# Kernel tuning notes

Measured on AMD Instinct MI355X. Metric: run time of the kernel, lower is better.

Reference implementation:

```python
import jax, jax.numpy as jnp
import numpy as np

EPS = 1e-15
BALL_EPS = 1e-5  # geoopt-style clamp away from the ball boundary


def expmap0(u):
    # Poincare ball (curvature -1): expmap0(u) = tanh(||u||) * u / ||u||
    n = jnp.linalg.norm(u, axis=-1, keepdims=True)
    n = jnp.maximum(n, EPS)
    return jnp.tanh(n) * u / n


def setup_inputs() -> dict:
    key = jax.random.key(0)
    k1, k2, k3 = jax.random.split(key, 3)
    B, H, D, L = 32768, 768, 384, 128
    cls_output = jax.random.normal(k1, (B, H), dtype=jnp.float32)
    W_proj = jax.random.normal(k2, (H, D), dtype=jnp.float32) * 0.02
    b_proj = jnp.zeros((D,), dtype=jnp.float32)
    # class prototypes: uniform(-0.1, 0.1) then expmap0, as in __init__
    tangent = jax.random.uniform(k3, (L, D), dtype=jnp.float32, minval=-0.1, maxval=0.1)
    poincare_weight = expmap0(tangent)
    return {"cls_output": cls_output, "W_proj": W_proj, "b_proj": b_proj,
            "poincare_weight": poincare_weight}


def reference(cls_output, W_proj, b_proj, poincare_weight):
    # projection (dropout is identity in eval mode)
    projected = cls_output @ W_proj + b_proj            # [B, D]
    x = expmap0(projected)                              # [B, D] points in ball
    y = poincare_weight                                 # [L, D] class reps in ball
    # Poincare distance for all (B, L) pairs, fused via dot products:
    # ||(-x) mobius+ y||^2 = ||x - y||^2 / (1 - 2<x,y> + ||x||^2 ||y||^2)
    x2 = jnp.sum(x * x, axis=-1)                        # [B]
    y2 = jnp.sum(y * y, axis=-1)                        # [L]
    xy = x @ y.T                                        # [B, L]
    sq_diff = x2[:, None] + y2[None, :] - 2.0 * xy      # ||x - y||^2
    denom = 1.0 - 2.0 * xy + x2[:, None] * y2[None, :]
    ratio = jnp.clip(sq_diff / denom, 0.0, (1.0 - BALL_EPS) ** 2)
    dist = 2.0 * jnp.arctanh(jnp.sqrt(ratio))           # [B, L]
    logits = -dist
    return logits, x
```

## Files before the change

kernel.cpp:

```cpp
#include <hip/hip_runtime.h>

typedef __attribute__((ext_vector_type(8))) short bf16x8;
typedef __attribute__((ext_vector_type(16))) float f32x16;

__device__ __forceinline__ unsigned short f2b(float f) {
  unsigned x = __builtin_bit_cast(unsigned, f);
  x += 0x7fffu + ((x >> 16) & 1u);
  return (unsigned short)(x >> 16);
}

__global__ __launch_bounds__(256) void k_prep(const float* __restrict__ W,
                                              const float* __restrict__ Y,
                                              unsigned short* __restrict__ Wt,
                                              unsigned short* __restrict__ Ybf,
                                              float* __restrict__ y2) {
  __shared__ unsigned short sT[64][72];
  int b = blockIdx.x;
  if (b < 72) {
    int bk = (b % 12) * 64, bn = (b / 12) * 64;
    int c = threadIdx.x & 63, rr = threadIdx.x >> 6;
#pragma unroll
    for (int i = 0; i < 16; i++) {
      int row = rr * 16 + i;
      sT[row][c] = f2b(W[(size_t)(bk + row) * 384 + bn + c]);
    }
    __syncthreads();
#pragma unroll
    for (int i = 0; i < 16; i++) {
      int row = rr * 16 + i;
      Wt[(size_t)(bn + row) * 768 + bk + c] = sT[c][row];
    }
  } else {
    int t = threadIdx.x;
    for (int i = t; i < 12288; i += 256) {
      float4 v = ((const float4*)Y)[i];
      ushort4 o;
      o.x = f2b(v.x); o.y = f2b(v.y); o.z = f2b(v.z); o.w = f2b(v.w);
      ((ushort4*)Ybf)[i] = o;
    }
    if (t < 128) {
      const float4* row = (const float4*)(Y + (size_t)t * 384);
      float s = 0.f;
#pragma unroll
      for (int j = 0; j < 96; j++) {
        float4 v = row[j];
        s += v.x * v.x + v.y * v.y + v.z * v.z + v.w * v.w;
      }
      y2[t] = s;
    }
  }
}

#define LDS1 72

__global__ __launch_bounds__(512, 2) void k_proj(const float* __restrict__ cls,
                                                 const unsigned short* __restrict__ Wt,
                                                 const float* __restrict__ bias,
                                                 float* __restrict__ xout,
                                                 float* __restrict__ x2out) {
  __shared__ unsigned short sA[128 * LDS1];
  __shared__ unsigned short sW[384 * LDS1];
  __shared__ float rs[128][4];
  __shared__ float sF[128];

  const int tid = threadIdx.x;
  const int bm = blockIdx.x * 128;
  const int wave = tid >> 6, lane = tid & 63;
  const int r = lane & 31, h = lane >> 5;
  const int rg = wave & 1, cg = wave >> 1;

  f32x16 acc[2][3];
#pragma unroll
  for (int i = 0; i < 2; i++)
#pragma unroll
    for (int j = 0; j < 3; j++)
#pragma unroll
      for (int e = 0; e < 16; e++) acc[i][j][e] = 0.f;

  for (int k0 = 0; k0 < 768; k0 += 64) {
    __syncthreads();
#pragma unroll
    for (int c = tid; c < 1024; c += 512) {
      int row = c >> 3, kc = c & 7;
      const float* src = cls + (size_t)(bm + row) * 768 + k0 + kc * 8;
      float4 f0 = *(const float4*)(src);
      float4 f1 = *(const float4*)(src + 4);
      uint4 p;
      p.x = (unsigned)f2b(f0.x) | ((unsigned)f2b(f0.y) << 16);
      p.y = (unsigned)f2b(f0.z) | ((unsigned)f2b(f0.w) << 16);
      p.z = (unsigned)f2b(f1.x) | ((unsigned)f2b(f1.y) << 16);
      p.w = (unsigned)f2b(f1.z) | ((unsigned)f2b(f1.w) << 16);
      *(uint4*)(sA + row * LDS1 + kc * 8) = p;
    }
#pragma unroll
    for (int c = tid; c < 3072; c += 512) {
      int row = c >> 3, kc = c & 7;
      *(uint4*)(sW + row * LDS1 + kc * 8) =
          *(const uint4*)(Wt + (size_t)row * 768 + k0 + kc * 8);
    }
    __syncthreads();
#pragma unroll
    for (int sub = 0; sub < 4; sub++) {
      const int kk = sub * 16 + h * 8;
      bf16x8 a0 = *(const bf16x8*)(sA + (rg * 64 + r) * LDS1 + kk);
      bf16x8 a1 = *(const bf16x8*)(sA + (rg * 64 + 32 + r) * LDS1 + kk);
      bf16x8 b0 = *(const bf16x8*)(sW + (cg * 96 + r) * LDS1 + kk);
      bf16x8 b1 = *(const bf16x8*)(sW + (cg * 96 + 32 + r) * LDS1 + kk);
      bf16x8 b2 = *(const bf16x8*)(sW + (cg * 96 + 64 + r) * LDS1 + kk);
      acc[0][0] = __builtin_amdgcn_mfma_f32_32x32x16_bf16(a0, b0, acc[0][0], 0, 0, 0);
      acc[0][1] = __builtin_amdgcn_mfma_f32_32x32x16_bf16(a0, b1, acc[0][1], 0, 0, 0);
      acc[0][2] = __builtin_amdgcn_mfma_f32_32x32x16_bf16(a0, b2, acc[0][2], 0, 0, 0);
      acc[1][0] = __builtin_amdgcn_mfma_f32_32x32x16_bf16(a1, b0, acc[1][0], 0, 0, 0);
      acc[1][1] = __builtin_amdgcn_mfma_f32_32x32x16_bf16(a1, b1, acc[1][1], 0, 0, 0);
      acc[1][2] = __builtin_amdgcn_mfma_f32_32x32x16_bf16(a1, b2, acc[1][2], 0, 0, 0);
    }
  }

  float bcol[3];
#pragma unroll
  for (int j = 0; j < 3; j++) bcol[j] = bias[cg * 96 + j * 32 + r];

#pragma unroll
  for (int i = 0; i < 2; i++) {
#pragma unroll
    for (int reg = 0; reg < 16; reg++) {
      float s = 0.f;
#pragma unroll
      for (int j = 0; j < 3; j++) {
        float v = acc[i][j][reg] + bcol[j];
        acc[i][j][reg] = v;
        s += v * v;
      }
      s += __shfl_xor(s, 1);
      s += __shfl_xor(s, 2);
      s += __shfl_xor(s, 4);
      s += __shfl_xor(s, 8);
      s += __shfl_xor(s, 16);
      if (r == 0) {
        int rowl = rg * 64 + i * 32 + (reg & 3) + 8 * (reg >> 2) + 4 * h;
        rs[rowl][cg] = s;
      }
    }
  }
  __syncthreads();
  if (tid < 128) {
    float n2 = rs[tid][0] + rs[tid][1] + rs[tid][2] + rs[tid][3];
    float n = fmaxf(sqrtf(n2), 1e-15f);
    float f = tanhf(n) / n;
    sF[tid] = f;
    x2out[bm + tid] = n2 * f * f;
  }
  __syncthreads();
#pragma unroll
  for (int i = 0; i < 2; i++) {
#pragma unroll
    for (int reg = 0; reg < 16; reg++) {
      int rowl = rg * 64 + i * 32 + (reg & 3) + 8 * (reg >> 2) + 4 * h;
      float f = sF[rowl];
#pragma unroll
      for (int j = 0; j < 3; j++) {
        xout[(size_t)(bm + rowl) * 384 + cg * 96 + j * 32 + r] = acc[i][j][reg] * f;
      }
    }
  }
}

#define LDS2 136

__global__ __launch_bounds__(512, 4) void k_logits(const float* __restrict__ X,
                                                   const float* __restrict__ x2,
                                                   const unsigned short* __restrict__ Y,
                                                   const float* __restrict__ y2,
                                                   float* __restrict__ out) {
  __shared__ unsigned short sX[128 * LDS2];
  __shared__ unsigned short sY[128 * LDS2];
  const int tid = threadIdx.x;
  const int bm = blockIdx.x * 128;
  const int wave = tid >> 6, lane = tid & 63;
  const int r = lane & 31, h = lane >> 5;
  const int rt = 32 * (wave & 3), ct = 64 * (wave >> 2);

  f32x16 acc[2];
#pragma unroll
  for (int j = 0; j < 2; j++)
#pragma unroll
    for (int e = 0; e < 16; e++) acc[j][e] = 0.f;

  for (int k0 = 0; k0 < 384; k0 += 128) {
    __syncthreads();
#pragma unroll
    for (int c = tid; c < 2048; c += 512) {
      int row = c >> 4, kc = c & 15;
      const float* src = X + (size_t)(bm + row) * 384 + k0 + kc * 8;
      float4 f0 = *(const float4*)(src);
      float4 f1 = *(const float4*)(src + 4);
      uint4 p;
      p.x = (unsigned)f2b(f0.x) | ((unsigned)f2b(f0.y) << 16);
      p.y = (unsigned)f2b(f0.z) | ((unsigned)f2b(f0.w) << 16);
      p.z = (unsigned)f2b(f1.x) | ((unsigned)f2b(f1.y) << 16);
      p.w = (unsigned)f2b(f1.z) | ((unsigned)f2b(f1.w) << 16);
      *(uint4*)(sX + row * LDS2 + kc * 8) = p;
    }
#pragma unroll
    for (int c = tid; c < 2048; c += 512) {
      int row = c >> 4, kc = c & 15;
      *(uint4*)(sY + row * LDS2 + kc * 8) =
          *(const uint4*)(Y + (size_t)row * 384 + k0 + kc * 8);
    }
    __syncthreads();
#pragma unroll
    for (int sub = 0; sub < 8; sub++) {
      const int kk = sub * 16 + h * 8;
      bf16x8 a = *(const bf16x8*)(sX + (rt + r) * LDS2 + kk);
      bf16x8 b0 = *(const bf16x8*)(sY + (ct + r) * LDS2 + kk);
      bf16x8 b1 = *(const bf16x8*)(sY + (ct + 32 + r) * LDS2 + kk);
      acc[0] = __builtin_amdgcn_mfma_f32_32x32x16_bf16(a, b0, acc[0], 0, 0, 0);
      acc[1] = __builtin_amdgcn_mfma_f32_32x32x16_bf16(a, b1, acc[1], 0, 0, 0);
    }
  }

  const float CLIP = 0.9999800001f;
  float yc[2] = {y2[ct + r], y2[ct + 32 + r]};
#pragma unroll
  for (int reg = 0; reg < 16; reg++) {
    int rowl = rt + (reg & 3) + 8 * (reg >> 2) + 4 * h;
    float xr = x2[bm + rowl];
#pragma unroll
    for (int j = 0; j < 2; j++) {
      float xy = acc[j][reg];
      float sq = xr + yc[j] - 2.f * xy;
      float den = 1.f - 2.f * xy + xr * yc[j];
      float ratio = fminf(fmaxf(sq / den, 0.f), CLIP);
      float s = sqrtf(ratio);
      float dist = logf((1.f + s) / (1.f - s));
      out[(size_t)(bm + rowl) * 128 + ct + j * 32 + r] = -dist;
    }
  }
}

extern "C" void kernel_launch(void* const* d_in, const int* in_sizes, int n_in,
                              void* d_out, int out_size, void* d_ws, size_t ws_size,
                              hipStream_t stream) {
  const float* cls  = (const float*)d_in[0];
  const float* W    = (const float*)d_in[1];
  const float* bias = (const float*)d_in[2];
  const float* Y    = (const float*)d_in[3];

  float* out_logits = (float*)d_out;
  float* out_x = out_logits + (size_t)32768 * 128;

  float* x2 = (float*)d_ws;
  float* y2 = x2 + 32768;
  unsigned short* Wt = (unsigned short*)(y2 + 128);
  unsigned short* Ybf = Wt + (size_t)384 * 768;

  k_prep<<<73, 256, 0, stream>>>(W, Y, Wt, Ybf, y2);
  k_proj<<<256, 512, 0, stream>>>(cls, Wt, bias, out_x, x2);
  k_logits<<<256, 512, 0, stream>>>(out_x, x2, Ybf, y2, out_logits);
}
```

Baseline: 232.3 us.

## Fuse projection and logits kernels, keep x in LDS, prefetch GEMM tiles in registers

Merges k_proj and k_logits into a single kernel. The normalized x tile is written as bf16 into shared memory and x2 stays in shared memory, so the second GEMM no longer re-reads x from global memory or launches a separate kernel. The first GEMM loop now prefetches the next K tile of cls and Wt into registers while the current tile is computed, and uses raw barriers instead of __syncthreads. The fused kernel needs a larger shared allocation (~135KB) plus more registers, which may reduce occupancy.

```diff
diff --git a/kernel.cpp b/kernel.cpp
--- a/kernel.cpp
+++ b/kernel.cpp
@@ -52,16 +52,25 @@
 }
 
 #define LDS1 72
-
-__global__ __launch_bounds__(512, 2) void k_proj(const float* __restrict__ cls,
+#define LDSX 392
+#define LDSY 136
+
+__global__ __launch_bounds__(512, 2) void k_main(const float* __restrict__ cls,
                                                  const unsigned short* __restrict__ Wt,
                                                  const float* __restrict__ bias,
+                                                 const unsigned short* __restrict__ Ybf,
+                                                 const float* __restrict__ y2,
                                                  float* __restrict__ xout,
-                                                 float* __restrict__ x2out) {
-  __shared__ unsigned short sA[128 * LDS1];
-  __shared__ unsigned short sW[384 * LDS1];
+                                                 float* __restrict__ out) {
+  __shared__ __align__(16) unsigned short sm[50176 + 17408];
   __shared__ float rs[128][4];
   __shared__ float sF[128];
+  __shared__ float sQ[128];
+
+  unsigned short* sA = sm;
+  unsigned short* sW = sm + 9216;
+  unsigned short* sX = sm;
+  unsigned short* sY = sm + 50176;
 
   const int tid = threadIdx.x;
   const int bm = blockIdx.x * 128;
@@ -77,28 +86,61 @@
 #pragma unroll
       for (int e = 0; e < 16; e++) acc[i][j][e] = 0.f;
 
-  for (int k0 = 0; k0 < 768; k0 += 64) {
-    __syncthreads();
-#pragma unroll
-    for (int c = tid; c < 1024; c += 512) {
-      int row = c >> 3, kc = c & 7;
-      const float* src = cls + (size_t)(bm + row) * 768 + k0 + kc * 8;
-      float4 f0 = *(const float4*)(src);
-      float4 f1 = *(const float4*)(src + 4);
+  float4 rA[2][2];
+  uint4 rW[6];
+
+#pragma unroll
+  for (int it = 0; it < 2; it++) {
+    int c = tid + it * 512, row = c >> 3, kc = c & 7;
+    const float* src = cls + (size_t)(bm + row) * 768 + kc * 8;
+    rA[it][0] = *(const float4*)(src);
+    rA[it][1] = *(const float4*)(src + 4);
+  }
+#pragma unroll
+  for (int it = 0; it < 6; it++) {
+    int c = tid + it * 512, row = c >> 3, kc = c & 7;
+    rW[it] = *(const uint4*)(Wt + (size_t)row * 768 + kc * 8);
+  }
+
+  for (int t = 0; t < 12; t++) {
+    asm volatile("s_waitcnt lgkmcnt(0)" ::: "memory");
+    __builtin_amdgcn_s_barrier();
+
+#pragma unroll
+    for (int it = 0; it < 2; it++) {
+      int c = tid + it * 512, row = c >> 3, kc = c & 7;
       uint4 p;
-      p.x = (unsigned)f2b(f0.x) | ((unsigned)f2b(f0.y) << 16);
-      p.y = (unsigned)f2b(f0.z) | ((unsigned)f2b(f0.w) << 16);
-      p.z = (unsigned)f2b(f1.x) | ((unsigned)f2b(f1.y) << 16);
-      p.w = (unsigned)f2b(f1.z) | ((unsigned)f2b(f1.w) << 16);
+      p.x = (unsigned)f2b(rA[it][0].x) | ((unsigned)f2b(rA[it][0].y) << 16);
+      p.y = (unsigned)f2b(rA[it][0].z) | ((unsigned)f2b(rA[it][0].w) << 16);
+      p.z = (unsigned)f2b(rA[it][1].x) | ((unsigned)f2b(rA[it][1].y) << 16);
+      p.w = (unsigned)f2b(rA[it][1].z) | ((unsigned)f2b(rA[it][1].w) << 16);
       *(uint4*)(sA + row * LDS1 + kc * 8) = p;
     }
 #pragma unroll
-    for (int c = tid; c < 3072; c += 512) {
-      int row = c >> 3, kc = c & 7;
-      *(uint4*)(sW + row * LDS1 + kc * 8) =
-          *(const uint4*)(Wt + (size_t)row * 768 + k0 + kc * 8);
-    }
-    __syncthreads();
+    for (int it = 0; it < 6; it++) {
+      int c = tid + it * 512, row = c >> 3, kc = c & 7;
+      *(uint4*)(sW + row * LDS1 + kc * 8) = rW[it];
+    }
+
+    if (t < 11) {
+      const int k0 = (t + 1) * 64;
+#pragma unroll
+      for (int it = 0; it < 2; it++) {
+        int c = tid + it * 512, row = c >> 3, kc = c & 7;
+        const float* src = cls + (size_t)(bm + row) * 768 + k0 + kc * 8;
+        rA[it][0] = *(const float4*)(src);
+        rA[it][1] = *(const float4*)(src + 4);
+      }
+#pragma unroll
+      for (int it = 0; it < 6; it++) {
+        int c = tid + it * 512, row = c >> 3, kc = c & 7;
+        rW[it] = *(const uint4*)(Wt + (size_t)row * 768 + k0 + kc * 8);
+      }
+    }
+
+    asm volatile("s_waitcnt lgkmcnt(0)" ::: "memory");
+    __builtin_amdgcn_s_barrier();
+
 #pragma unroll
     for (int sub = 0; sub < 4; sub++) {
       const int kk = sub * 16 + h * 8;
@@ -148,9 +190,10 @@
     float n = fmaxf(sqrtf(n2), 1e-15f);
     float f = tanhf(n) / n;
     sF[tid] = f;
-    x2out[bm + tid] = n2 * f * f;
+    sQ[tid] = n2 * f * f;
   }
   __syncthreads();
+
 #pragma unroll
   for (int i = 0; i < 2; i++) {
 #pragma unroll
@@ -159,63 +202,39 @@
       float f = sF[rowl];
 #pragma unroll
       for (int j = 0; j < 3; j++) {
-        xout[(size_t)(bm + rowl) * 384 + cg * 96 + j * 32 + r] = acc[i][j][reg] * f;
-      }
-    }
-  }
-}
-
-#define LDS2 136
-
-__global__ __launch_bounds__(512, 4) void k_logits(const float* __restrict__ X,
-                                                   const float* __restrict__ x2,
-                                                   const unsigned short* __restrict__ Y,
-                                                   const float* __restrict__ y2,
-                                                   float* __restrict__ out) {
-  __shared__ unsigned short sX[128 * LDS2];
-  __shared__ unsigned short sY[128 * LDS2];
-  const int tid = threadIdx.x;
-  const int bm = blockIdx.x * 128;
-  const int wave = tid >> 6, lane = tid & 63;
-  const int r = lane & 31, h = lane >> 5;
+        float v = acc[i][j][reg] * f;
+        xout[(size_t)(bm + rowl) * 384 + cg * 96 + j * 32 + r] = v;
+        sX[rowl * LDSX + cg * 96 + j * 32 + r] = f2b(v);
+      }
+    }
+  }
+
   const int rt = 32 * (wave & 3), ct = 64 * (wave >> 2);
-
-  f32x16 acc[2];
+  f32x16 acc2[2];
 #pragma unroll
   for (int j = 0; j < 2; j++)
 #pragma unroll
-    for (int e = 0; e < 16; e++) acc[j][e] = 0.f;
+    for (int e = 0; e < 16; e++) acc2[j][e] = 0.f;
 
   for (int k0 = 0; k0 < 384; k0 += 128) {
-    __syncthreads();
+    asm volatile("s_waitcnt lgkmcnt(0)" ::: "memory");
+    __builtin_amdgcn_s_barrier();
 #pragma unroll
     for (int c = tid; c < 2048; c += 512) {
       int row = c >> 4, kc = c & 15;
-      const float* src = X + (size_t)(bm + row) * 384 + k0 + kc * 8;
-      float4 f0 = *(const float4*)(src);
-      float4 f1 = *(const float4*)(src + 4);
-      uint4 p;
-      p.x = (unsigned)f2b(f0.x) | ((unsigned)f2b(f0.y) << 16);
-      p.y = (unsigned)f2b(f0.z) | ((unsigned)f2b(f0.w) << 16);
-      p.z = (unsigned)f2b(f1.x) | ((unsigned)f2b(f1.y) << 16);
-      p.w = (unsigned)f2b(f1.z) | ((unsigned)f2b(f1.w) << 16);
-      *(uint4*)(sX + row * LDS2 + kc * 8) = p;
-    }
-#pragma unroll
-    for (int c = tid; c < 2048; c += 512) {
-      int row = c >> 4, kc = c & 15;
-      *(uint4*)(sY + row * LDS2 + kc * 8) =
-          *(const uint4*)(Y + (size_t)row * 384 + k0 + kc * 8);
-    }
-    __syncthreads();
+      *(uint4*)(sY + row * LDSY + kc * 8) =
+          *(const uint4*)(Ybf + (size_t)row * 384 + k0 + kc * 8);
+    }
+    asm volatile("s_waitcnt lgkmcnt(0)" ::: "memory");
+    __builtin_amdgcn_s_barrier();
 #pragma unroll
     for (int sub = 0; sub < 8; sub++) {
       const int kk = sub * 16 + h * 8;
-      bf16x8 a = *(const bf16x8*)(sX + (rt + r) * LDS2 + kk);
-      bf16x8 b0 = *(const bf16x8*)(sY + (ct + r) * LDS2 + kk);
-      bf16x8 b1 = *(const bf16x8*)(sY + (ct + 32 + r) * LDS2 + kk);
-      acc[0] = __builtin_amdgcn_mfma_f32_32x32x16_bf16(a, b0, acc[0], 0, 0, 0);
-      acc[1] = __builtin_amdgcn_mfma_f32_32x32x16_bf16(a, b1, acc[1], 0, 0, 0);
+      bf16x8 a = *(const bf16x8*)(sX + (rt + r) * LDSX + k0 + kk);
+      bf16x8 b0 = *(const bf16x8*)(sY + (ct + r) * LDSY + kk);
+      bf16x8 b1 = *(const bf16x8*)(sY + (ct + 32 + r) * LDSY + kk);
+      acc2[0] = __builtin_amdgcn_mfma_f32_32x32x16_bf16(a, b0, acc2[0], 0, 0, 0);
+      acc2[1] = __builtin_amdgcn_mfma_f32_32x32x16_bf16(a, b1, acc2[1], 0, 0, 0);
     }
   }
 
@@ -224,10 +243,10 @@
 #pragma unroll
   for (int reg = 0; reg < 16; reg++) {
     int rowl = rt + (reg & 3) + 8 * (reg >> 2) + 4 * h;
-    float xr = x2[bm + rowl];
+    float xr = sQ[rowl];
 #pragma unroll
     for (int j = 0; j < 2; j++) {
-      float xy = acc[j][reg];
+      float xy = acc2[j][reg];
       float sq = xr + yc[j] - 2.f * xy;
       float den = 1.f - 2.f * xy + xr * yc[j];
       float ratio = fminf(fmaxf(sq / den, 0.f), CLIP);
@@ -255,6 +274,5 @@
   unsigned short* Ybf = Wt + (size_t)384 * 768;
 
   k_prep<<<73, 256, 0, stream>>>(W, Y, Wt, Ybf, y2);
-  k_proj<<<256, 512, 0, stream>>>(cls, Wt, bias, out_x, x2);
-  k_logits<<<256, 512, 0, stream>>>(out_x, x2, Ybf, y2, out_logits);
-}
+  k_main<<<256, 512, 0, stream>>>(cls, Wt, bias, Ybf, y2, out_x, out_logits);
+}
```

Result: slower. 240.1 us (+3.3%).
